# Kernel optimization log

Hardware: AMD Instinct MI355X
Metric: run time of the kernel (lower is better)

The kernel has to match this reference:

```python
import jax, jax.numpy as jnp
import numpy as np


def _unpack_int4(packed):
    """Unpack bytes (stored as int32 in [0,256)) into signed int4 values in [-8,7].
    packed: [..., K/2] -> [..., K], low nibble first."""
    lo = packed & 0xF
    hi = (packed >> 4) & 0xF
    lo = lo - 16 * (lo >= 8).astype(jnp.int32)
    hi = hi - 16 * (hi >= 8).astype(jnp.int32)
    out = jnp.stack([lo, hi], axis=-1)
    return out.reshape(packed.shape[:-1] + (packed.shape[-1] * 2,))


def setup_inputs() -> dict:
    key = jax.random.key(0)
    ks = jax.random.split(key, 7)
    M, K, N, R = 8192, 4096, 4096, 32
    return {
        "x_quant": jax.random.randint(ks[0], (M, K // 2), 0, 256, dtype=jnp.int32),
        "x_scale": jax.random.uniform(ks[1], (M,), dtype=jnp.float32) * 0.01 + 1e-3,
        "weight": jax.random.randint(ks[2], (N, K // 2), 0, 256, dtype=jnp.int32),
        "weight_scales": jax.random.uniform(ks[3], (N,), dtype=jnp.float32) * 0.01 + 1e-3,
        "bias": jax.random.normal(ks[4], (N,), dtype=jnp.float32) * 0.01,
        "x_r": jax.random.normal(ks[5], (M, R), dtype=jnp.float32),
        "w_outlier": jax.random.normal(ks[6], (N, R), dtype=jnp.float32),
    }


def reference(x_quant, x_scale, weight, weight_scales, bias, x_r, w_outlier):
    # Unpack packed int4 operands: [M,K] and [N,K], values in [-8,7]
    xq = _unpack_int4(x_quant)
    wq = _unpack_int4(weight)
    # Integer GEMM (s4s4 accumulate in int32), then fused dequant + bias
    acc = jnp.matmul(xq, wq.T)  # [M, N] int32
    out = acc.astype(jnp.float32) * x_scale[:, None] * weight_scales[None, :] + bias[None, :]
    # Low-rank outlier correction: addmm_(x_r, w_outlier.T)
    out = out + jnp.matmul(x_r, w_outlier.T)
    return out
```

## Files before the change

### kernel.cpp

```cpp
#include <hip/hip_runtime.h>

#define M_ 8192
#define K_ 4096
#define N_ 4096
#define R_ 32
#define KP_ (K_ / 2)

#define BM 256
#define BN 256
#define BK 64
#define NT (K_ / BK)
#define NBUF 4
#define ABUF_SZ 16384
#define TILE_SZ 32768
#define GRID ((M_ / BM) * (N_ / BN))

typedef __attribute__((ext_vector_type(4))) int    i32x4;
typedef __attribute__((ext_vector_type(4))) float  f32x4;
typedef __attribute__((ext_vector_type(8))) __bf16 bf16x8;

__device__ __forceinline__ void gload16(const void* g, void* l) {
  __builtin_amdgcn_global_load_lds(
      (const __attribute__((address_space(1))) unsigned int*)g,
      (__attribute__((address_space(3))) unsigned int*)l, 16, 0, 0);
}

__device__ __forceinline__ unsigned nib2(int b) {
  unsigned lo = (unsigned)(((b & 15) ^ 8) - 8) & 0xFFu;
  unsigned hi = (unsigned)((((b >> 4) & 15) ^ 8) - 8) & 0xFFu;
  return lo | (hi << 8);
}

__global__ void repack_int4(const int* __restrict__ in, unsigned* __restrict__ out, int n4) {
  int stride = gridDim.x * blockDim.x;
  for (int i = blockIdx.x * blockDim.x + threadIdx.x; i < n4; i += stride) {
    int4 v = ((const int4*)in)[i];
    uint2 o;
    o.x = nib2(v.x) | (nib2(v.y) << 16);
    o.y = nib2(v.z) | (nib2(v.w) << 16);
    ((uint2*)out)[i] = o;
  }
}

__device__ __forceinline__ unsigned short f2b(float x) {
  unsigned u = __float_as_uint(x);
  return (unsigned short)((u + 0x7FFFu + ((u >> 16) & 1u)) >> 16);
}

__global__ void f2bf4(const float* __restrict__ in, unsigned short* __restrict__ out, int n4) {
  int stride = gridDim.x * blockDim.x;
  for (int i = blockIdx.x * blockDim.x + threadIdx.x; i < n4; i += stride) {
    float4 f = ((const float4*)in)[i];
    ushort4 o;
    o.x = f2b(f.x); o.y = f2b(f.y); o.z = f2b(f.z); o.w = f2b(f.w);
    ((ushort4*)out)[i] = o;
  }
}

__global__ __launch_bounds__(512, 2) void gemm_w4a4(
    const signed char* __restrict__ x8, const signed char* __restrict__ w8,
    const unsigned short* __restrict__ xrb, const unsigned short* __restrict__ wob,
    const float* __restrict__ xscale, const float* __restrict__ wscale,
    const float* __restrict__ bias, float* __restrict__ out)
{
  extern __shared__ __align__(16) char lds[];

  const int t    = threadIdx.x;
  const int w    = t >> 6;
  const int l    = t & 63;
  const int lrow = l & 15;
  const int lgrp = l >> 4;
  const int wr   = w >> 2;
  const int wc   = w & 3;

  const int swz  = (blockIdx.x & 7) * (GRID / 8) + (blockIdx.x >> 3);
  const int m0   = (swz & 31) * BM;
  const int n0   = (swz >> 5) * BN;

  const signed char* aS0 = x8 + (size_t)(m0 + w * 16 + lrow) * K_ + lgrp * 16;
  const signed char* aS1 = x8 + (size_t)(m0 + (8 + w) * 16 + lrow) * K_ + lgrp * 16;
  const signed char* bS0 = w8 + (size_t)(n0 + w * 16 + lrow) * K_ + lgrp * 16;
  const signed char* bS1 = w8 + (size_t)(n0 + (8 + w) * 16 + lrow) * K_ + lgrp * 16;

#define STAGE_A(tile)                                                        \
  { char* d = lds + ((tile) & 3) * TILE_SZ + w * 1024;                       \
    gload16(aS0 + (size_t)(tile) * BK, d);                                   \
    gload16(aS1 + (size_t)(tile) * BK, d + 8192); }
#define STAGE_B(tile)                                                        \
  { char* d = lds + ((tile) & 3) * TILE_SZ + ABUF_SZ + w * 1024;             \
    gload16(bS0 + (size_t)(tile) * BK, d);                                   \
    gload16(bS1 + (size_t)(tile) * BK, d + 8192); }
#define FENCE asm volatile("" ::: "memory")

  i32x4 acc[8][4] = {};

  STAGE_A(0) STAGE_B(0)
  STAGE_A(1) STAGE_B(1)
  STAGE_A(2) STAGE_B(2)
  asm volatile("s_waitcnt vmcnt(8)" ::: "memory");
  __builtin_amdgcn_s_barrier();
  FENCE;

  for (int kt = 0; kt < NT; ++kt) {
    const char* Ab = lds + (kt & 3) * TILE_SZ;
    const char* Bb = Ab + ABUF_SZ;

    i32x4 bf[4], af0[4];
    #pragma unroll
    for (int n = 0; n < 4; ++n)
      bf[n] = *(const i32x4*)(Bb + (wc * 4 + n) * 1024 + l * 16);
    #pragma unroll
    for (int m = 0; m < 4; ++m)
      af0[m] = *(const i32x4*)(Ab + (wr * 8 + m) * 1024 + l * 16);
    if (kt < NT - 3) STAGE_A(kt + 3)
    FENCE;
    __builtin_amdgcn_s_barrier();
    FENCE;
    __builtin_amdgcn_s_setprio(1);
    #pragma unroll
    for (int m = 0; m < 4; ++m)
      #pragma unroll
      for (int n = 0; n < 4; ++n)
        acc[m][n] = __builtin_amdgcn_mfma_i32_16x16x64_i8(af0[m], bf[n], acc[m][n], 0, 0, 0);
    __builtin_amdgcn_s_setprio(0);
    FENCE;
    __builtin_amdgcn_s_barrier();
    FENCE;

    i32x4 af1[4];
    #pragma unroll
    for (int m = 0; m < 4; ++m)
      af1[m] = *(const i32x4*)(Ab + (wr * 8 + 4 + m) * 1024 + l * 16);
    if (kt < NT - 3) {
      STAGE_B(kt + 3)
      asm volatile("s_waitcnt vmcnt(8)" ::: "memory");
    } else if (kt == NT - 3) {
      asm volatile("s_waitcnt vmcnt(4)" ::: "memory");
    } else if (kt == NT - 2) {
      asm volatile("s_waitcnt vmcnt(0)" ::: "memory");
    }
    FENCE;
    __builtin_amdgcn_s_barrier();
    FENCE;
    __builtin_amdgcn_s_setprio(1);
    #pragma unroll
    for (int m = 0; m < 4; ++m)
      #pragma unroll
      for (int n = 0; n < 4; ++n)
        acc[4 + m][n] = __builtin_amdgcn_mfma_i32_16x16x64_i8(af1[m], bf[n], acc[4 + m][n], 0, 0, 0);
    __builtin_amdgcn_s_setprio(0);
    FENCE;
    __builtin_amdgcn_s_barrier();
    FENCE;
  }

  f32x4 sxv[8];
  #pragma unroll
  for (int m = 0; m < 8; ++m)
    sxv[m] = *(const f32x4*)(xscale + m0 + wr * 128 + m * 16 + lgrp * 4);
  float swv[4], bv[4];
  #pragma unroll
  for (int n = 0; n < 4; ++n) {
    int cg = n0 + wc * 64 + n * 16 + lrow;
    swv[n] = wscale[cg];
    bv[n]  = bias[cg];
  }
  bf16x8 ar[8], br[4];
  #pragma unroll
  for (int m = 0; m < 8; ++m)
    ar[m] = *(const bf16x8*)(xrb + (size_t)(m0 + wr * 128 + m * 16 + lrow) * R_ + lgrp * 8);
  #pragma unroll
  for (int n = 0; n < 4; ++n)
    br[n] = *(const bf16x8*)(wob + (size_t)(n0 + wc * 64 + n * 16 + lrow) * R_ + lgrp * 8);

  #pragma unroll
  for (int m = 0; m < 8; ++m) {
    #pragma unroll
    for (int n = 0; n < 4; ++n) {
      f32x4 z = {0.0f, 0.0f, 0.0f, 0.0f};
      f32x4 c = __builtin_amdgcn_mfma_f32_16x16x32_bf16(ar[m], br[n], z, 0, 0, 0);
      #pragma unroll
      for (int j = 0; j < 4; ++j) {
        int rg = m0 + wr * 128 + m * 16 + lgrp * 4 + j;
        int cg = n0 + wc * 64 + n * 16 + lrow;
        out[(size_t)rg * N_ + cg] =
            (float)acc[m][n][j] * sxv[m][j] * swv[n] + c[j] + bv[n];
      }
    }
  }
}

extern "C" void kernel_launch(void* const* d_in, const int* in_sizes, int n_in,
                              void* d_out, int out_size, void* d_ws, size_t ws_size,
                              hipStream_t stream) {
  const int*   x_quant   = (const int*)d_in[0];
  const float* x_scale   = (const float*)d_in[1];
  const int*   weight    = (const int*)d_in[2];
  const float* w_scales  = (const float*)d_in[3];
  const float* bias      = (const float*)d_in[4];
  const float* x_r       = (const float*)d_in[5];
  const float* w_outlier = (const float*)d_in[6];
  float* out = (float*)d_out;

  char* ws = (char*)d_ws;
  signed char*    x8  = (signed char*)ws;
  signed char*    w8  = (signed char*)(ws + (size_t)M_ * K_);
  unsigned short* xrb = (unsigned short*)(ws + (size_t)M_ * K_ + (size_t)N_ * K_);
  unsigned short* wob = xrb + (size_t)M_ * R_;

  (void)hipFuncSetAttribute((const void*)gemm_w4a4,
                            hipFuncAttributeMaxDynamicSharedMemorySize,
                            NBUF * TILE_SZ);

  repack_int4<<<2048, 256, 0, stream>>>(x_quant, (unsigned*)x8, M_ * KP_ / 4);
  repack_int4<<<2048, 256, 0, stream>>>(weight,  (unsigned*)w8, N_ * KP_ / 4);
  f2bf4<<<256, 256, 0, stream>>>(x_r, xrb, M_ * R_ / 4);
  f2bf4<<<128, 256, 0, stream>>>(w_outlier, wob, N_ * R_ / 4);

  gemm_w4a4<<<GRID, 512, NBUF * TILE_SZ, stream>>>(
      x8, w8, xrb, wob, x_scale, w_scales, bias, out);
}
```

Measured before the change: 183.0 us.

## Repack int4 operands into tile-contiguous layout for coalesced LDS staging

```diff
diff --git a/kernel.cpp b/kernel.cpp
--- a/kernel.cpp
+++ b/kernel.cpp
@@ -10,8 +10,7 @@
 #define BN 256
 #define BK 64
 #define NT (K_ / BK)
-#define NBUF 4
-#define ABUF_SZ 16384
+#define ATILE 16384
 #define TILE_SZ 32768
 #define GRID ((M_ / BM) * (N_ / BN))
 
@@ -31,14 +30,24 @@
   return lo | (hi << 8);
 }
 
-__global__ void repack_int4(const int* __restrict__ in, unsigned* __restrict__ out, int n4) {
-  int stride = gridDim.x * blockDim.x;
-  for (int i = blockIdx.x * blockDim.x + threadIdx.x; i < n4; i += stride) {
-    int4 v = ((const int4*)in)[i];
-    uint2 o;
-    o.x = nib2(v.x) | (nib2(v.y) << 16);
-    o.y = nib2(v.z) | (nib2(v.w) << 16);
-    ((uint2*)out)[i] = o;
+__global__ void repack_tiled(const int* __restrict__ in, uint4* __restrict__ out) {
+  const int tile = blockIdx.x;
+  const int rt = tile >> 6, kt = tile & 63;
+  const int t = threadIdx.x;
+  #pragma unroll
+  for (int i = 0; i < 4; ++i) {
+    int g = t + i * 256;
+    int u = g >> 6, l = g & 63;
+    int row = rt * 256 + u * 16 + (l & 15);
+    int w0  = kt * 32 + (l >> 4) * 8;
+    const int4* p = (const int4*)(in + (size_t)row * KP_ + w0);
+    int4 a = p[0], b = p[1];
+    uint4 o;
+    o.x = nib2(a.x) | (nib2(a.y) << 16);
+    o.y = nib2(a.z) | (nib2(a.w) << 16);
+    o.z = nib2(b.x) | (nib2(b.y) << 16);
+    o.w = nib2(b.z) | (nib2(b.w) << 16);
+    out[(size_t)tile * 1024 + g] = o;
   }
 }
 
@@ -58,7 +67,7 @@
 }
 
 __global__ __launch_bounds__(512, 2) void gemm_w4a4(
-    const signed char* __restrict__ x8, const signed char* __restrict__ w8,
+    const char* __restrict__ x8t, const char* __restrict__ w8t,
     const unsigned short* __restrict__ xrb, const unsigned short* __restrict__ wob,
     const float* __restrict__ xscale, const float* __restrict__ wscale,
     const float* __restrict__ bias, float* __restrict__ out)
@@ -73,23 +82,21 @@
   const int wr   = w >> 2;
   const int wc   = w & 3;
 
-  const int swz  = (blockIdx.x & 7) * (GRID / 8) + (blockIdx.x >> 3);
-  const int m0   = (swz & 31) * BM;
-  const int n0   = (swz >> 5) * BN;
-
-  const signed char* aS0 = x8 + (size_t)(m0 + w * 16 + lrow) * K_ + lgrp * 16;
-  const signed char* aS1 = x8 + (size_t)(m0 + (8 + w) * 16 + lrow) * K_ + lgrp * 16;
-  const signed char* bS0 = w8 + (size_t)(n0 + w * 16 + lrow) * K_ + lgrp * 16;
-  const signed char* bS1 = w8 + (size_t)(n0 + (8 + w) * 16 + lrow) * K_ + lgrp * 16;
-
-#define STAGE_A(tile)                                                        \
-  { char* d = lds + ((tile) & 3) * TILE_SZ + w * 1024;                       \
-    gload16(aS0 + (size_t)(tile) * BK, d);                                   \
-    gload16(aS1 + (size_t)(tile) * BK, d + 8192); }
-#define STAGE_B(tile)                                                        \
-  { char* d = lds + ((tile) & 3) * TILE_SZ + ABUF_SZ + w * 1024;             \
-    gload16(bS0 + (size_t)(tile) * BK, d);                                   \
-    gload16(bS1 + (size_t)(tile) * BK, d + 8192); }
+  const int swz = (blockIdx.x & 7) * (GRID / 8) + (blockIdx.x >> 3);
+  const int mt  = swz & 31, nt = swz >> 5;
+  const int m0  = mt * BM, n0 = nt * BN;
+
+  const char* aT = x8t + (size_t)mt * NT * ATILE;
+  const char* bT = w8t + (size_t)nt * NT * ATILE;
+
+#define STAGE_A(tile)                                                         \
+  { const char* s = aT + (size_t)(tile) * ATILE + w * 1024 + (l) * 16;        \
+    char* d = lds + ((tile) & 3) * TILE_SZ + w * 1024;                        \
+    gload16(s, d); gload16(s + 8192, d + 8192); }
+#define STAGE_B(tile)                                                         \
+  { const char* s = bT + (size_t)(tile) * ATILE + w * 1024 + (l) * 16;        \
+    char* d = lds + ((tile) & 3) * TILE_SZ + ATILE + w * 1024;                \
+    gload16(s, d); gload16(s + 8192, d + 8192); }
 #define FENCE asm volatile("" ::: "memory")
 
   i32x4 acc[8][4] = {};
@@ -103,7 +110,7 @@
 
   for (int kt = 0; kt < NT; ++kt) {
     const char* Ab = lds + (kt & 3) * TILE_SZ;
-    const char* Bb = Ab + ABUF_SZ;
+    const char* Bb = Ab + ATILE;
 
     i32x4 bf[4], af0[4];
     #pragma unroll
@@ -203,20 +210,20 @@
   float* out = (float*)d_out;
 
   char* ws = (char*)d_ws;
-  signed char*    x8  = (signed char*)ws;
-  signed char*    w8  = (signed char*)(ws + (size_t)M_ * K_);
+  char*           x8t = ws;
+  char*           w8t = ws + (size_t)M_ * K_;
   unsigned short* xrb = (unsigned short*)(ws + (size_t)M_ * K_ + (size_t)N_ * K_);
   unsigned short* wob = xrb + (size_t)M_ * R_;
 
   (void)hipFuncSetAttribute((const void*)gemm_w4a4,
                             hipFuncAttributeMaxDynamicSharedMemorySize,
-                            NBUF * TILE_SZ);
-
-  repack_int4<<<2048, 256, 0, stream>>>(x_quant, (unsigned*)x8, M_ * KP_ / 4);
-  repack_int4<<<2048, 256, 0, stream>>>(weight,  (unsigned*)w8, N_ * KP_ / 4);
+                            4 * TILE_SZ);
+
+  repack_tiled<<<(M_ / BM) * NT, 256, 0, stream>>>(x_quant, (uint4*)x8t);
+  repack_tiled<<<(N_ / BN) * NT, 256, 0, stream>>>(weight,  (uint4*)w8t);
   f2bf4<<<256, 256, 0, stream>>>(x_r, xrb, M_ * R_ / 4);
   f2bf4<<<128, 256, 0, stream>>>(w_outlier, wob, N_ * R_ / 4);
 
-  gemm_w4a4<<<GRID, 512, NBUF * TILE_SZ, stream>>>(
-      x8, w8, xrb, wob, x_scale, w_scales, bias, out);
-}
+  gemm_w4a4<<<GRID, 512, 4 * TILE_SZ, stream>>>(
+      x8t, w8t, xrb, wob, x_scale, w_scales, bias, out);
+}
```

Result: faster. 170.1 us (-7.1%).
